# Optimization experiments

Measured on AMD Instinct MI355X. Metric: run time of the kernel, lower is better.

The kernel has to match this reference:

```python
import jax, jax.numpy as jnp
import numpy as np

RADIUS = 5.0
CORRECT_THRESHOLD = 0.5
NUM_CLASSES = 4
COORD_RANGE = 64.0  # keep coords in a small field so some preds actually match


def setup_inputs() -> dict:
    key = jax.random.key(0)
    k1, k2, k3, k4 = jax.random.split(key, 4)
    B, P, T = 16, 4096, 1024
    pred_cls = jax.random.randint(k1, (B, P, 1), 0, NUM_CLASSES).astype(jnp.float32)
    pred_xy = jax.random.uniform(k2, (B, P, 2), dtype=jnp.float32) * COORD_RANGE
    gt_cls = jax.random.randint(k3, (B, T, 1), 0, NUM_CLASSES).astype(jnp.float32)
    gt_xy = jax.random.uniform(k4, (B, T, 2), dtype=jnp.float32) * COORD_RANGE
    pred = jnp.concatenate([pred_cls, pred_xy], axis=-1)  # [B,P,3]
    gt = jnp.concatenate([gt_cls, gt_xy], axis=-1)        # [B,T,3]
    return {"pred": pred, "gt": gt}


def _radial_score(centers, targets):
    # centers: [B,P,2], targets: [B,T,2] -> [B,P,T]; sigmoid(1 - dist/radius)
    d = centers[:, :, None, :] - targets[:, None, :, :]
    dist = jnp.sqrt(jnp.sum(d * d, axis=-1))
    return jax.nn.sigmoid(1.0 - dist / RADIUS)


def reference(pred, gt):
    B, P, _ = pred.shape
    T = gt.shape[1]
    classes = pred[:, :, 0]          # [B,P]
    centers = pred[:, :, 1:3]        # [B,P,2]
    tclasses = gt[:, :, 0]           # [B,T]
    tcenters = gt[:, :, 1:3]         # [B,T,2]

    scores = _radial_score(centers, tcenters)                       # [B,P,T]
    valid = (scores >= CORRECT_THRESHOLD) & (
        classes[:, :, None] == tclasses[:, None, :])                # [B,P,T]

    # Greedy dedup (sort-by-score + unique on target col) keeps, per target,
    # its highest-scoring valid pred; the second unique (pred col) only drops
    # duplicate preds and never changes the set of matched pred indices.
    masked = jnp.where(valid, scores, -jnp.inf)
    best_pred = jnp.argmax(masked, axis=1)                          # [B,T]
    has_match = jnp.any(valid, axis=1)                              # [B,T]

    flat_idx = (best_pred + jnp.arange(B, dtype=best_pred.dtype)[:, None] * P).ravel()
    hits = jnp.zeros((B * P,), jnp.float32).at[flat_idx].add(
        has_match.ravel().astype(jnp.float32))
    correct = hits.reshape(B, P) > 0                                # [B,P]

    tp = correct.sum().astype(jnp.float32)
    fp = jnp.float32(B * P) - tp
    fn = jnp.float32(B * T) - tp

    eps = jnp.float32(1e-6)
    precision = (tp + eps) / (tp + eps + fp + eps)
    recall = (tp + eps) / (tp + fn + eps)
    f1 = 2.0 * precision * recall / (precision + recall)
    return 1.0 - f1
```

## Files before the change

kernel.cpp:

```cpp
#include <hip/hip_runtime.h>
#include <math.h>

#define BB 16
#define PP 4096
#define TT 1024
#define JT 8
#define SENT 0xFFFFFFFFu

__global__ __launch_bounds__(256) void match_kernel(const float* __restrict__ pred,
                                                    const float* __restrict__ gt,
                                                    unsigned int* __restrict__ best) {
    const int blk   = blockIdx.x;
    const int b     = blk >> 5;
    const int ttile = blk & 31;
    const int wave  = threadIdx.x >> 6;
    const int lane  = threadIdx.x & 63;
    const int tbase = ttile * 32 + wave * JT;

    const float* gb = gt + ((size_t)(b * TT + tbase)) * 3;
    float gc[JT], gx[JT], gy[JT], bd[JT];
    unsigned int bp[JT];
    #pragma unroll
    for (int j = 0; j < JT; ++j) {
        gc[j] = gb[j * 3 + 0];
        gx[j] = gb[j * 3 + 1];
        gy[j] = gb[j * 3 + 2];
        bd[j] = INFINITY;
        bp[j] = SENT;
    }

    const float* pl = pred + (size_t)b * PP * 3 + lane * 3;

    #pragma unroll 2
    for (int i = 0; i < PP / 64; ++i) {
        const float pc = pl[0];
        const float px = pl[1];
        const float py = pl[2];
        pl += 64 * 3;
        const unsigned int p = (unsigned int)(lane + (i << 6));
        #pragma unroll
        for (int j = 0; j < JT; ++j) {
            const float dx = px - gx[j];
            const float dy = py - gy[j];
            const float d2 = fmaf(dx, dx, dy * dy);
            const bool ok = (pc == gc[j]) & (d2 <= 25.0f) & (d2 < bd[j]);
            if (ok) { bd[j] = d2; bp[j] = p; }
        }
    }

    unsigned long long key[JT];
    #pragma unroll
    for (int j = 0; j < JT; ++j)
        key[j] = ((unsigned long long)__float_as_uint(bd[j]) << 32) | bp[j];

    for (int off = 32; off; off >>= 1) {
        #pragma unroll
        for (int j = 0; j < JT; ++j) {
            const unsigned long long o = __shfl_down(key[j], off, 64);
            if (o < key[j]) key[j] = o;
        }
    }

    if (lane == 0) {
        #pragma unroll
        for (int j = 0; j < JT; ++j)
            best[b * TT + tbase + j] = (unsigned int)key[j];
    }
}

__global__ __launch_bounds__(1024) void count_kernel(const unsigned int* __restrict__ best,
                                                     float* __restrict__ out) {
    __shared__ unsigned int bm[BB * PP / 32];
    for (int i = threadIdx.x; i < BB * PP / 32; i += 1024) bm[i] = 0;
    __syncthreads();

    const uint4* b4 = (const uint4*)best;
    for (int i = threadIdx.x; i < (BB * TT / 4); i += 1024) {
        const uint4 v = b4[i];
        const int t0 = i * 4;
        const unsigned int vs[4] = {v.x, v.y, v.z, v.w};
        #pragma unroll
        for (int k = 0; k < 4; ++k) {
            if (vs[k] != SENT) {
                const unsigned int g = (unsigned int)((t0 + k) >> 10) * PP + vs[k];
                atomicOr(&bm[g >> 5], 1u << (g & 31));
            }
        }
    }
    __syncthreads();

    int sum = 0;
    for (int i = threadIdx.x; i < BB * PP / 32; i += 1024) sum += __popc(bm[i]);
    for (int off = 32; off; off >>= 1) sum += __shfl_down(sum, off, 64);

    __shared__ int ss[16];
    const int wid  = threadIdx.x >> 6;
    const int lane = threadIdx.x & 63;
    if (lane == 0) ss[wid] = sum;
    __syncthreads();
    if (threadIdx.x == 0) {
        int tp_i = 0;
        for (int w = 0; w < 16; ++w) tp_i += ss[w];
        const float tp = (float)tp_i;
        const float eps = 1e-6f;
        const float fp = (float)(BB * PP) - tp;
        const float fn = (float)(BB * TT) - tp;
        const float precision = (tp + eps) / (tp + eps + fp + eps);
        const float recall    = (tp + eps) / (tp + fn + eps);
        const float f1 = 2.0f * precision * recall / (precision + recall);
        out[0] = 1.0f - f1;
    }
}

extern "C" void kernel_launch(void* const* d_in, const int* in_sizes, int n_in,
                              void* d_out, int out_size, void* d_ws, size_t ws_size,
                              hipStream_t stream) {
    const float* pred = (const float*)d_in[0];
    const float* gt   = (const float*)d_in[1];
    float* out = (float*)d_out;
    unsigned int* best = (unsigned int*)d_ws;

    match_kernel<<<BB * TT / 32, 256, 0, stream>>>(pred, gt, best);
    count_kernel<<<1, 1024, 0, stream>>>(best, out);
}
```

Measured before the change: 85.37 us.

## Split pred range across two blocks and defer radius check to merge

Each match block now scans only half of the predictions, doubling the grid from 512 to 1024 blocks, and writes 64-bit (dist,index) partial keys per half. The count kernel merges the two halves by min and applies the radius threshold there, removing the per-candidate radius compare from the inner loop. The pred loads are software-pipelined one iteration ahead. In exchange the workspace is larger and the count kernel reads twice as much data as 64-bit values.

After: 76.08 us. 1.12x faster.

```diff
diff --git a/kernel.cpp b/kernel.cpp
--- a/kernel.cpp
+++ b/kernel.cpp
@@ -5,14 +5,16 @@
 #define PP 4096
 #define TT 1024
 #define JT 8
+#define HALF 2048
 #define SENT 0xFFFFFFFFu
 
 __global__ __launch_bounds__(256) void match_kernel(const float* __restrict__ pred,
                                                     const float* __restrict__ gt,
-                                                    unsigned int* __restrict__ best) {
+                                                    unsigned long long* __restrict__ part) {
     const int blk   = blockIdx.x;
-    const int b     = blk >> 5;
-    const int ttile = blk & 31;
+    const int b     = blk >> 6;
+    const int ttile = (blk >> 1) & 31;
+    const int half  = blk & 1;
     const int wave  = threadIdx.x >> 6;
     const int lane  = threadIdx.x & 63;
     const int tbase = ttile * 32 + wave * JT;
@@ -29,21 +31,33 @@
         bp[j] = SENT;
     }
 
-    const float* pl = pred + (size_t)b * PP * 3 + lane * 3;
+    const int pbase = half * HALF;
+    const float* pl = pred + (size_t)b * PP * 3 + (size_t)(pbase + lane) * 3;
 
-    #pragma unroll 2
-    for (int i = 0; i < PP / 64; ++i) {
-        const float pc = pl[0];
-        const float px = pl[1];
-        const float py = pl[2];
-        pl += 64 * 3;
-        const unsigned int p = (unsigned int)(lane + (i << 6));
+    float c0 = pl[0], x0 = pl[1], y0 = pl[2];
+    #pragma unroll 4
+    for (int i = 0; i < HALF / 64 - 1; ++i) {
+        pl += 192;
+        const float c1 = pl[0], x1 = pl[1], y1 = pl[2];
+        const unsigned int p = (unsigned int)(pbase + (i << 6) + lane);
         #pragma unroll
         for (int j = 0; j < JT; ++j) {
-            const float dx = px - gx[j];
-            const float dy = py - gy[j];
+            const float dx = x0 - gx[j];
+            const float dy = y0 - gy[j];
             const float d2 = fmaf(dx, dx, dy * dy);
-            const bool ok = (pc == gc[j]) & (d2 <= 25.0f) & (d2 < bd[j]);
+            const bool ok = (c0 == gc[j]) & (d2 < bd[j]);
+            if (ok) { bd[j] = d2; bp[j] = p; }
+        }
+        c0 = c1; x0 = x1; y0 = y1;
+    }
+    {
+        const unsigned int p = (unsigned int)(pbase + HALF - 64 + lane);
+        #pragma unroll
+        for (int j = 0; j < JT; ++j) {
+            const float dx = x0 - gx[j];
+            const float dy = y0 - gy[j];
+            const float d2 = fmaf(dx, dx, dy * dy);
+            const bool ok = (c0 == gc[j]) & (d2 < bd[j]);
             if (ok) { bd[j] = d2; bp[j] = p; }
         }
     }
@@ -64,27 +78,24 @@
     if (lane == 0) {
         #pragma unroll
         for (int j = 0; j < JT; ++j)
-            best[b * TT + tbase + j] = (unsigned int)key[j];
+            part[(size_t)half * (BB * TT) + b * TT + tbase + j] = key[j];
     }
 }
 
-__global__ __launch_bounds__(1024) void count_kernel(const unsigned int* __restrict__ best,
+__global__ __launch_bounds__(1024) void count_kernel(const unsigned long long* __restrict__ part,
                                                      float* __restrict__ out) {
     __shared__ unsigned int bm[BB * PP / 32];
     for (int i = threadIdx.x; i < BB * PP / 32; i += 1024) bm[i] = 0;
     __syncthreads();
 
-    const uint4* b4 = (const uint4*)best;
-    for (int i = threadIdx.x; i < (BB * TT / 4); i += 1024) {
-        const uint4 v = b4[i];
-        const int t0 = i * 4;
-        const unsigned int vs[4] = {v.x, v.y, v.z, v.w};
-        #pragma unroll
-        for (int k = 0; k < 4; ++k) {
-            if (vs[k] != SENT) {
-                const unsigned int g = (unsigned int)((t0 + k) >> 10) * PP + vs[k];
-                atomicOr(&bm[g >> 5], 1u << (g & 31));
-            }
+    const unsigned int lim = __float_as_uint(25.0f);
+    for (int i = threadIdx.x; i < BB * TT; i += 1024) {
+        unsigned long long k0 = part[i];
+        unsigned long long k1 = part[(size_t)(BB * TT) + i];
+        const unsigned long long k = k0 < k1 ? k0 : k1;
+        if ((unsigned int)(k >> 32) <= lim) {
+            const unsigned int g = (unsigned int)(i >> 10) * PP + (unsigned int)k;
+            atomicOr(&bm[g >> 5], 1u << (g & 31));
         }
     }
     __syncthreads();
@@ -118,8 +129,8 @@
     const float* pred = (const float*)d_in[0];
     const float* gt   = (const float*)d_in[1];
     float* out = (float*)d_out;
-    unsigned int* best = (unsigned int*)d_ws;
+    unsigned long long* part = (unsigned long long*)d_ws;
 
-    match_kernel<<<BB * TT / 32, 256, 0, stream>>>(pred, gt, best);
-    count_kernel<<<1, 1024, 0, stream>>>(best, out);
+    match_kernel<<<BB * TT / 32 * 2, 256, 0, stream>>>(pred, gt, part);
+    count_kernel<<<1, 1024, 0, stream>>>(part, out);
 }
```
